# Performance work log

Measured on AMD Instinct MI355X. Metric: run time of the kernel, lower is better.

Reference implementation:

```python
import jax, jax.numpy as jnp
import numpy as np
import math

EPS = 1e-07
ALPHA = 0.2
FINAL_LAMBDA = 0.01   # final_beta in the original
ITERATIONS = 2
MEAN_DATA = 1.0

B, H, W, KH, KW, I, O, A = 16, 6, 6, 3, 3, 32, 32, 4


def setup_inputs() -> dict:
    key = jax.random.key(0)
    k1, k2 = jax.random.split(key)
    votes = jax.random.normal(k1, (B, H, W, KH, KW, I, O, A, A), dtype=jnp.float32)
    activations = jax.random.uniform(k2, (B, H, W, KH, KW, I, 1, 1, 1), dtype=jnp.float32)
    beta_a = jnp.full((1, 1, 1, 1, 1, 1, O, 1, 1), 0.5, dtype=jnp.float32)
    beta_u = jnp.full((1, 1, 1, 1, 1, 1, O, 1, 1), 0.5, dtype=jnp.float32)
    return {"votes": votes, "activations": activations, "beta_a": beta_a, "beta_u": beta_u}


def _m_step(a_i, V, R, R_prev, beta_a, beta_u, it_idx):
    # R mixing with previous assignments (faithful to source)
    R = R * a_i * (1.0 - ALPHA) + ALPHA * R_prev
    R_prev = R
    # reduce over kernel (3,4) and input-capsule (5) axes
    sum_R = jnp.sum(R, axis=(3, 4, 5), keepdims=True)                      # (b,h,w,1,1,1,o,1,1)
    mu = jnp.sum(R * V, axis=(3, 4, 5), keepdims=True) / (sum_R + EPS)     # (b,h,w,1,1,1,o,a,a)
    sigma_sq = jnp.sum(R * (V - mu) ** 2, axis=(3, 4, 5), keepdims=True) / (sum_R + EPS)
    cost_h = (beta_u - 0.5 * jnp.log(sigma_sq + EPS)) * sum_R / MEAN_DATA
    inv_temp = FINAL_LAMBDA * (1.0 - 0.95 ** (it_idx + 1))
    a_j = jax.nn.sigmoid(inv_temp * (beta_a - jnp.sum(cost_h, axis=(-1, -2), keepdims=True)))
    return mu, sigma_sq, a_j, R_prev


def _e_step_log(V, mu, sigma_sq, a_j):
    # log-space E-step: log N(V; mu, sigma) summed over the 4x4 pose entries
    log_p = -jnp.sum(jnp.log(2.0 * math.pi * sigma_sq + EPS) + (V - mu) ** 2 / (2.0 * sigma_sq),
                     axis=(-1, -2), keepdims=True)                         # (b,h,w,kh,kw,i,o,1,1)
    log_num = jnp.log(a_j + EPS) + log_p
    log_den = jax.scipy.special.logsumexp(log_num, axis=(3, 4, 6), keepdims=True)
    return jnp.exp(log_num - log_den)


def reference(votes, activations, beta_a, beta_u):
    b, h, w, kh, kw, i, o, a, _ = votes.shape
    # softmax over zeros along axis 6 -> uniform 1/o
    R = jnp.full((b, h, w, 1, 1, i, o, 1, 1), 1.0 / o, dtype=votes.dtype)
    R_prev = R
    mu = sigma_sq = a_j = None
    for it in range(ITERATIONS - 1):
        mu, sigma_sq, a_j, R_prev = _m_step(activations, votes, R, R_prev, beta_a, beta_u, it)
        R = _e_step_log(votes, mu, sigma_sq, a_j)
    # final M-step called with i = iterations (matches source)
    mu, sigma_sq, a_j, R_prev = _m_step(activations, votes, R, R_prev, beta_a, beta_u, ITERATIONS)
    poses = jnp.squeeze(mu, axis=(3, 4, 5))   # (b,h,w,o,a,a)
    acts = jnp.squeeze(a_j, axis=(3, 4, 5))   # (b,h,w,o,1,1)
    return poses, acts
```

## Files before the change

kernel.cpp:

```cpp
#include <hip/hip_runtime.h>


#define KKc 9
#define NIc 32
#define NOc 32
#define NAc 16
#define KIc 288
#define KOc 288
#define NPc 512
#define MSTR 17

__device__ __forceinline__ float wave_sum(float v) {
#pragma unroll
  for (int off = 32; off; off >>= 1) v += __shfl_down(v, off, 64);
  return v;
}
__device__ __forceinline__ float wave_max(float v) {
#pragma unroll
  for (int off = 32; off; off >>= 1) v = fmaxf(v, __shfl_down(v, off, 64));
  return v;
}

__global__ __launch_bounds__(256, 4)
void em_routing_kernel(const float* __restrict__ votes,
                       const float* __restrict__ acts_in,
                       const float* __restrict__ beta_a,
                       const float* __restrict__ beta_u,
                       float* __restrict__ out, int nsite)
{
  const int site = blockIdx.x;
  const int t    = threadIdx.x;
  const float EPSf  = 1e-7f;
  const float TWO_PI = 6.28318530717958647692f;

  __shared__ float s_VT[NAc * KOc];
  __shared__ float s_act[KIc];
  __shared__ float s_mu1[NOc * MSTR];
  __shared__ float s_lt1[NOc * MSTR];
  __shared__ float s_i2s[NOc * MSTR];
  __shared__ float s_m1v[NOc * MSTR];
  __shared__ float s_m1q[NOc * MSTR];
  __shared__ float s_laj[NOc];
  __shared__ float s_ln[KOc];
  __shared__ float s_w[KOc];
  __shared__ float s_sR2[NOc];
  __shared__ float s_red[4];
  __shared__ float s_red2[256];

  const float* vsite = votes + (size_t)site * (KIc * NPc);

  s_act[t] = acts_in[site * KIc + t];
  if (t < KIc - 256) s_act[t + 256] = acts_in[site * KIc + t + 256];
  __syncthreads();

  float sumR1;
  {
    float v = fmaf(0.8f, s_act[t], 0.2f);
    if (t < KIc - 256) v += fmaf(0.8f, s_act[t + 256], 0.2f);
    v = wave_sum(v);
    if ((t & 63) == 0) s_red[t >> 6] = v;
    __syncthreads();
    sumR1 = (s_red[0] + s_red[1] + s_red[2] + s_red[3]) * 0.03125f;
    __syncthreads();
  }

  float p1v0 = 0.f, p1v1 = 0.f, p1q0 = 0.f, p1q1 = 0.f;
#pragma unroll 4
  for (int ki = 0; ki < KIc; ++ki) {
    const float r = fmaf(0.8f, s_act[ki], 0.2f) * 0.03125f;
    const float2 v = *reinterpret_cast<const float2*>(vsite + ki * NPc + 2 * t);
    p1v0 = fmaf(r, v.x, p1v0);
    p1q0 = fmaf(r, v.x * v.x, p1q0);
    p1v1 = fmaf(r, v.y, p1v1);
    p1q1 = fmaf(r, v.y * v.y, p1q1);
  }
  {
    const int o1  = t >> 3;
    const int a2a = (t & 7) * 2;
    const float sR1e = sumR1 + EPSf;
    const float mua = p1v0 / sR1e;
    const float mub = p1v1 / sR1e;
    const float sga = fmaxf((p1q0 - mua * mua * (sumR1 + 2.f * EPSf)) / sR1e, 0.f);
    const float sgb = fmaxf((p1q1 - mub * mub * (sumR1 + 2.f * EPSf)) / sR1e, 0.f);
    const int b = o1 * MSTR + a2a;
    s_mu1[b]     = mua;  s_mu1[b + 1] = mub;
    s_lt1[b]     = logf(TWO_PI * sga + EPSf);
    s_lt1[b + 1] = logf(TWO_PI * sgb + EPSf);
    s_i2s[b]     = 0.5f / sga;
    s_i2s[b + 1] = 0.5f / sgb;
    s_m1v[b] = p1v0; s_m1v[b + 1] = p1v1;
    s_m1q[b] = p1q0; s_m1q[b + 1] = p1q1;
    const float bu = beta_u[o1];
    float ch = (bu - 0.5f * logf(sga + EPSf)) * sumR1
             + (bu - 0.5f * logf(sgb + EPSf)) * sumR1;
#pragma unroll
    for (int off = 1; off < 8; off <<= 1) ch += __shfl_xor(ch, off, 64);
    if ((t & 7) == 0) {
      const float aj = 1.f / (1.f + expf(-(0.0005f * (beta_a[o1] - ch))));
      s_laj[o1] = logf(aj + EPSf);
    }
  }
  __syncthreads();

  float sR2acc = 0.f;
  float m2va = 0.f, m2vb = 0.f, m2qa = 0.f, m2qb = 0.f;
  const int oB  = t & 31;
  const int a2B = (t >> 5) * 2;

  for (int i = 0; i < NIc; ++i) {
    __syncthreads();
    for (int idx = t; idx < KKc * 128; idx += 256) {
      const int kk  = idx >> 7;
      const int rem = idx & 127;
      const int o   = rem >> 2;
      const int a4  = (rem & 3) * 4;
      const float4 v = reinterpret_cast<const float4*>(vsite)[(kk * NIc + i) * 128 + rem];
      s_VT[(a4 + 0) * KOc + kk * NOc + o] = v.x;
      s_VT[(a4 + 1) * KOc + kk * NOc + o] = v.y;
      s_VT[(a4 + 2) * KOc + kk * NOc + o] = v.z;
      s_VT[(a4 + 3) * KOc + kk * NOc + o] = v.w;
    }
    __syncthreads();

    float ln1, ln2 = -1e30f;
    {
      const int o  = t & 31;
      const int ob = o * MSTR;
      float lp = 0.f;
#pragma unroll
      for (int a2 = 0; a2 < NAc; ++a2) {
        const float d = s_VT[a2 * KOc + t] - s_mu1[ob + a2];
        lp += s_lt1[ob + a2] + d * d * s_i2s[ob + a2];
      }
      ln1 = s_laj[o] - lp;
      s_ln[t] = ln1;
    }
    if (t < KOc - 256) {
      const int idx = t + 256;
      const int o   = idx & 31;
      const int ob  = o * MSTR;
      float lp = 0.f;
#pragma unroll
      for (int a2 = 0; a2 < NAc; ++a2) {
        const float d = s_VT[a2 * KOc + idx] - s_mu1[ob + a2];
        lp += s_lt1[ob + a2] + d * d * s_i2s[ob + a2];
      }
      ln2 = s_laj[o] - lp;
      s_ln[idx] = ln2;
    }
    float m = wave_max(fmaxf(ln1, ln2));
    if ((t & 63) == 0) s_red[t >> 6] = m;
    __syncthreads();
    m = fmaxf(fmaxf(s_red[0], s_red[1]), fmaxf(s_red[2], s_red[3]));
    float e = expf(ln1 - m) + ((t < KOc - 256) ? expf(ln2 - m) : 0.f);
    e = wave_sum(e);
    __syncthreads();
    if ((t & 63) == 0) s_red[t >> 6] = e;
    __syncthreads();
    const float logden = m + logf(s_red[0] + s_red[1] + s_red[2] + s_red[3]);

    {
      const int kk = t >> 5;
      s_w[t] = expf(ln1 - logden) * s_act[kk * NIc + i] * 0.8f;
    }
    if (t < KOc - 256) {
      const int idx = t + 256;
      const int kk  = idx >> 5;
      s_w[idx] = expf(ln2 - logden) * s_act[kk * NIc + i] * 0.8f;
    }
    __syncthreads();

    if (t < NOc) {
      float sw = 0.f;
#pragma unroll
      for (int kk = 0; kk < KKc; ++kk) sw += s_w[kk * NOc + t];
      sR2acc += sw;
    }
#pragma unroll
    for (int kk = 0; kk < KKc; ++kk) {
      const int bb = kk * NOc + oB;
      const float w  = s_w[bb];
      const float va = s_VT[a2B * KOc + bb];
      const float vb = s_VT[(a2B + 1) * KOc + bb];
      m2va = fmaf(w, va, m2va);
      m2qa = fmaf(w, va * va, m2qa);
      m2vb = fmaf(w, vb, m2vb);
      m2qb = fmaf(w, vb * vb, m2qb);
    }
  }

  if (t < NOc) s_sR2[t] = sR2acc;
  __syncthreads();

  {
    const float sumR = s_sR2[oB] + 0.2f * sumR1;
    const float sRe  = sumR + EPSf;
    const int b = oB * MSTR + a2B;
    const float Mva = m2va + 0.2f * s_m1v[b];
    const float Mqa = m2qa + 0.2f * s_m1q[b];
    const float Mvb = m2vb + 0.2f * s_m1v[b + 1];
    const float Mqb = m2qb + 0.2f * s_m1q[b + 1];
    const float mua = Mva / sRe;
    const float mub = Mvb / sRe;
    const float sga = fmaxf((Mqa - mua * mua * (sumR + 2.f * EPSf)) / sRe, 0.f);
    const float sgb = fmaxf((Mqb - mub * mub * (sumR + 2.f * EPSf)) / sRe, 0.f);

    float* poses = out + (size_t)site * NPc;
    poses[oB * NAc + a2B]     = mua;
    poses[oB * NAc + a2B + 1] = mub;

    const float bu = beta_u[oB];
    const float ch = (bu - 0.5f * logf(sga + EPSf)) * sumR
                   + (bu - 0.5f * logf(sgb + EPSf)) * sumR;
    s_red2[t] = ch;
  }
  __syncthreads();
  if (t < NOc) {
    float c = 0.f;
#pragma unroll
    for (int k = 0; k < 8; ++k) c += s_red2[t + 32 * k];
    const float aj = 1.f / (1.f + expf(-(0.00142625f * (beta_a[t] - c))));
    out[(size_t)nsite * NPc + site * NOc + t] = aj;
  }
}

extern "C" void kernel_launch(void* const* d_in, const int* in_sizes, int n_in,
                              void* d_out, int out_size, void* d_ws, size_t ws_size,
                              hipStream_t stream) {
  const float* votes  = (const float*)d_in[0];
  const float* acts   = (const float*)d_in[1];
  const float* beta_a = (const float*)d_in[2];
  const float* beta_u = (const float*)d_in[3];
  float* out = (float*)d_out;
  const int nsite = 16 * 6 * 6;
  em_routing_kernel<<<nsite, 256, 0, stream>>>(votes, acts, beta_a, beta_u, out, nsite);
}
```

Before: 594.8 us.

## Split EM routing into three kernels to parallelize across input capsules

The single per-site kernel becomes three launches. The first computes the first M-step statistics with four blocks per site. The second runs the E-step and partial second M-step with eight blocks per site, each handling four input capsules. The third reduces the partials and writes poses and activations. This raises grid size from 576 blocks to thousands so the GPU has more parallelism. It also folds the log-sigma term into a per-output base constant and changes the shared-memory vote layout to pair-major with padding. The cost is workspace traffic, two extra launches, and a second full read of the votes.

```diff
diff --git a/kernel.cpp b/kernel.cpp
--- a/kernel.cpp
+++ b/kernel.cpp
@@ -8,7 +8,11 @@
 #define KIc 288
 #define KOc 288
 #define NPc 512
-#define MSTR 17
+#define NSITE 576
+#define VSTR 17
+
+#define EPSf 1e-7f
+#define TWO_PIf 6.28318530717958647692f
 
 __device__ __forceinline__ float wave_sum(float v) {
 #pragma unroll
@@ -21,132 +25,138 @@
   return v;
 }
 
-__global__ __launch_bounds__(256, 4)
-void em_routing_kernel(const float* __restrict__ votes,
-                       const float* __restrict__ acts_in,
-                       const float* __restrict__ beta_a,
-                       const float* __restrict__ beta_u,
-                       float* __restrict__ out, int nsite)
+__global__ __launch_bounds__(128)
+void em_k1(const float* __restrict__ votes, const float* __restrict__ acts_in,
+           const float* __restrict__ beta_a, const float* __restrict__ beta_u,
+           float* __restrict__ w_mu1, float* __restrict__ w_i2s,
+           float* __restrict__ w_m1v, float* __restrict__ w_m1q,
+           float* __restrict__ w_base, float* __restrict__ w_sR1)
 {
-  const int site = blockIdx.x;
+  const int site = blockIdx.x >> 2;
+  const int qtr  = blockIdx.x & 3;
   const int t    = threadIdx.x;
-  const float EPSf  = 1e-7f;
-  const float TWO_PI = 6.28318530717958647692f;
-
-  __shared__ float s_VT[NAc * KOc];
+  const int p    = qtr * 128 + t;
+
   __shared__ float s_act[KIc];
-  __shared__ float s_mu1[NOc * MSTR];
-  __shared__ float s_lt1[NOc * MSTR];
-  __shared__ float s_i2s[NOc * MSTR];
-  __shared__ float s_m1v[NOc * MSTR];
-  __shared__ float s_m1q[NOc * MSTR];
-  __shared__ float s_laj[NOc];
-  __shared__ float s_ln[KOc];
+  __shared__ float s_red[2];
+
+  s_act[t] = acts_in[site * KIc + t];
+  s_act[t + 128] = acts_in[site * KIc + t + 128];
+  if (t < 32) s_act[t + 256] = acts_in[site * KIc + t + 256];
+  __syncthreads();
+
+  float v = fmaf(0.8f, s_act[t], 0.2f) + fmaf(0.8f, s_act[t + 128], 0.2f);
+  if (t < 32) v += fmaf(0.8f, s_act[t + 256], 0.2f);
+  v = wave_sum(v);
+  if ((t & 63) == 0) s_red[t >> 6] = v;
+  __syncthreads();
+  const float sumR1 = (s_red[0] + s_red[1]) * 0.03125f;
+
+  float pv = 0.f, pq = 0.f;
+  const float* vs = votes + (size_t)site * (KIc * NPc) + p;
+#pragma unroll 8
+  for (int ki = 0; ki < KIc; ++ki) {
+    const float r = fmaf(0.8f, s_act[ki], 0.2f) * 0.03125f;
+    const float x = vs[(size_t)ki * NPc];
+    pv = fmaf(r, x, pv);
+    pq = fmaf(r, x * x, pq);
+  }
+
+  const int o = p >> 4;
+  const float sR1e = sumR1 + EPSf;
+  const float mu = pv / sR1e;
+  const float sg = fmaxf((pq - mu * mu * (sumR1 + 2.f * EPSf)) / sR1e, 0.f);
+
+  w_mu1[(size_t)site * NPc + p] = mu;
+  w_i2s[(size_t)site * NPc + p] = 0.5f / sg;
+  w_m1v[(size_t)site * NPc + p] = pv;
+  w_m1q[(size_t)site * NPc + p] = pq;
+
+  float lt = logf(TWO_PIf * sg + EPSf);
+  float ch = (beta_u[o] - 0.5f * logf(sg + EPSf)) * sumR1;
+#pragma unroll
+  for (int off = 1; off < 16; off <<= 1) {
+    ch += __shfl_xor(ch, off, 64);
+    lt += __shfl_xor(lt, off, 64);
+  }
+  if ((t & 15) == 0) {
+    const float aj = 1.f / (1.f + expf(-(0.0005f * (beta_a[o] - ch))));
+    w_base[site * NOc + o] = logf(aj + EPSf) - lt;
+  }
+  if (t == 0) w_sR1[site] = sumR1;
+}
+
+__global__ __launch_bounds__(256)
+void em_k3(const float* __restrict__ votes, const float* __restrict__ acts_in,
+           const float* __restrict__ w_mu1, const float* __restrict__ w_i2s,
+           const float* __restrict__ w_base,
+           float* __restrict__ w_m2v, float* __restrict__ w_m2q,
+           float* __restrict__ w_sR2)
+{
+  const int site = blockIdx.x >> 3;
+  const int ig   = blockIdx.x & 7;
+  const int t    = threadIdx.x;
+
+  __shared__ float s_V[KOc * VSTR];
+  __shared__ float s_mu[NOc * VSTR];
+  __shared__ float s_is[NOc * VSTR];
+  __shared__ float s_base[NOc];
+  __shared__ float s_act[KIc];
   __shared__ float s_w[KOc];
-  __shared__ float s_sR2[NOc];
   __shared__ float s_red[4];
-  __shared__ float s_red2[256];
-
-  const float* vsite = votes + (size_t)site * (KIc * NPc);
-
+
+  for (int idx = t; idx < NPc; idx += 256) {
+    const int o = idx >> 4, a2 = idx & 15;
+    s_mu[o * VSTR + a2] = w_mu1[(size_t)site * NPc + idx];
+    s_is[o * VSTR + a2] = w_i2s[(size_t)site * NPc + idx];
+  }
+  if (t < NOc) s_base[t] = w_base[site * NOc + t];
   s_act[t] = acts_in[site * KIc + t];
   if (t < KIc - 256) s_act[t + 256] = acts_in[site * KIc + t + 256];
-  __syncthreads();
-
-  float sumR1;
-  {
-    float v = fmaf(0.8f, s_act[t], 0.2f);
-    if (t < KIc - 256) v += fmaf(0.8f, s_act[t + 256], 0.2f);
-    v = wave_sum(v);
-    if ((t & 63) == 0) s_red[t >> 6] = v;
-    __syncthreads();
-    sumR1 = (s_red[0] + s_red[1] + s_red[2] + s_red[3]) * 0.03125f;
-    __syncthreads();
-  }
-
-  float p1v0 = 0.f, p1v1 = 0.f, p1q0 = 0.f, p1q1 = 0.f;
-#pragma unroll 4
-  for (int ki = 0; ki < KIc; ++ki) {
-    const float r = fmaf(0.8f, s_act[ki], 0.2f) * 0.03125f;
-    const float2 v = *reinterpret_cast<const float2*>(vsite + ki * NPc + 2 * t);
-    p1v0 = fmaf(r, v.x, p1v0);
-    p1q0 = fmaf(r, v.x * v.x, p1q0);
-    p1v1 = fmaf(r, v.y, p1v1);
-    p1q1 = fmaf(r, v.y * v.y, p1q1);
-  }
-  {
-    const int o1  = t >> 3;
-    const int a2a = (t & 7) * 2;
-    const float sR1e = sumR1 + EPSf;
-    const float mua = p1v0 / sR1e;
-    const float mub = p1v1 / sR1e;
-    const float sga = fmaxf((p1q0 - mua * mua * (sumR1 + 2.f * EPSf)) / sR1e, 0.f);
-    const float sgb = fmaxf((p1q1 - mub * mub * (sumR1 + 2.f * EPSf)) / sR1e, 0.f);
-    const int b = o1 * MSTR + a2a;
-    s_mu1[b]     = mua;  s_mu1[b + 1] = mub;
-    s_lt1[b]     = logf(TWO_PI * sga + EPSf);
-    s_lt1[b + 1] = logf(TWO_PI * sgb + EPSf);
-    s_i2s[b]     = 0.5f / sga;
-    s_i2s[b + 1] = 0.5f / sgb;
-    s_m1v[b] = p1v0; s_m1v[b + 1] = p1v1;
-    s_m1q[b] = p1q0; s_m1q[b + 1] = p1q1;
-    const float bu = beta_u[o1];
-    float ch = (bu - 0.5f * logf(sga + EPSf)) * sumR1
-             + (bu - 0.5f * logf(sgb + EPSf)) * sumR1;
-#pragma unroll
-    for (int off = 1; off < 8; off <<= 1) ch += __shfl_xor(ch, off, 64);
-    if ((t & 7) == 0) {
-      const float aj = 1.f / (1.f + expf(-(0.0005f * (beta_a[o1] - ch))));
-      s_laj[o1] = logf(aj + EPSf);
-    }
-  }
-  __syncthreads();
-
-  float sR2acc = 0.f;
-  float m2va = 0.f, m2vb = 0.f, m2qa = 0.f, m2qb = 0.f;
+
+  const float4* vsite4 = reinterpret_cast<const float4*>(votes + (size_t)site * (KIc * NPc));
+
+  float m2va = 0.f, m2vb = 0.f, m2qa = 0.f, m2qb = 0.f, sR2acc = 0.f;
   const int oB  = t & 31;
   const int a2B = (t >> 5) * 2;
 
-  for (int i = 0; i < NIc; ++i) {
-    __syncthreads();
-    for (int idx = t; idx < KKc * 128; idx += 256) {
+  for (int ii = 0; ii < 4; ++ii) {
+    const int i = ig * 4 + ii;
+    __syncthreads();
+    for (int idx = t; idx < 1152; idx += 256) {
       const int kk  = idx >> 7;
       const int rem = idx & 127;
-      const int o   = rem >> 2;
-      const int a4  = (rem & 3) * 4;
-      const float4 v = reinterpret_cast<const float4*>(vsite)[(kk * NIc + i) * 128 + rem];
-      s_VT[(a4 + 0) * KOc + kk * NOc + o] = v.x;
-      s_VT[(a4 + 1) * KOc + kk * NOc + o] = v.y;
-      s_VT[(a4 + 2) * KOc + kk * NOc + o] = v.z;
-      s_VT[(a4 + 3) * KOc + kk * NOc + o] = v.w;
+      const int pair = kk * NOc + (rem >> 2);
+      const int a4   = (rem & 3) * 4;
+      const float4 x = vsite4[(size_t)(kk * NIc + i) * 128 + rem];
+      s_V[pair * VSTR + a4 + 0] = x.x;
+      s_V[pair * VSTR + a4 + 1] = x.y;
+      s_V[pair * VSTR + a4 + 2] = x.z;
+      s_V[pair * VSTR + a4 + 3] = x.w;
     }
     __syncthreads();
 
     float ln1, ln2 = -1e30f;
     {
-      const int o  = t & 31;
-      const int ob = o * MSTR;
+      const int o = t & 31;
       float lp = 0.f;
 #pragma unroll
       for (int a2 = 0; a2 < NAc; ++a2) {
-        const float d = s_VT[a2 * KOc + t] - s_mu1[ob + a2];
-        lp += s_lt1[ob + a2] + d * d * s_i2s[ob + a2];
+        const float d = s_V[t * VSTR + a2] - s_mu[o * VSTR + a2];
+        lp = fmaf(d * d, s_is[o * VSTR + a2], lp);
       }
-      ln1 = s_laj[o] - lp;
-      s_ln[t] = ln1;
+      ln1 = s_base[o] - lp;
     }
     if (t < KOc - 256) {
       const int idx = t + 256;
-      const int o   = idx & 31;
-      const int ob  = o * MSTR;
+      const int o = idx & 31;
       float lp = 0.f;
 #pragma unroll
       for (int a2 = 0; a2 < NAc; ++a2) {
-        const float d = s_VT[a2 * KOc + idx] - s_mu1[ob + a2];
-        lp += s_lt1[ob + a2] + d * d * s_i2s[ob + a2];
+        const float d = s_V[idx * VSTR + a2] - s_mu[o * VSTR + a2];
+        lp = fmaf(d * d, s_is[o * VSTR + a2], lp);
       }
-      ln2 = s_laj[o] - lp;
-      s_ln[idx] = ln2;
+      ln2 = s_base[o] - lp;
     }
     float m = wave_max(fmaxf(ln1, ln2));
     if ((t & 63) == 0) s_red[t >> 6] = m;
@@ -159,15 +169,9 @@
     __syncthreads();
     const float logden = m + logf(s_red[0] + s_red[1] + s_red[2] + s_red[3]);
 
-    {
-      const int kk = t >> 5;
-      s_w[t] = expf(ln1 - logden) * s_act[kk * NIc + i] * 0.8f;
-    }
-    if (t < KOc - 256) {
-      const int idx = t + 256;
-      const int kk  = idx >> 5;
-      s_w[idx] = expf(ln2 - logden) * s_act[kk * NIc + i] * 0.8f;
-    }
+    s_w[t] = expf(ln1 - logden) * s_act[(t >> 5) * NIc + i] * 0.8f;
+    if (t < KOc - 256)
+      s_w[t + 256] = expf(ln2 - logden) * s_act[8 * NIc + i] * 0.8f;
     __syncthreads();
 
     if (t < NOc) {
@@ -180,8 +184,8 @@
     for (int kk = 0; kk < KKc; ++kk) {
       const int bb = kk * NOc + oB;
       const float w  = s_w[bb];
-      const float va = s_VT[a2B * KOc + bb];
-      const float vb = s_VT[(a2B + 1) * KOc + bb];
+      const float va = s_V[bb * VSTR + a2B];
+      const float vb = s_V[bb * VSTR + a2B + 1];
       m2va = fmaf(w, va, m2va);
       m2qa = fmaf(w, va * va, m2qa);
       m2vb = fmaf(w, vb, m2vb);
@@ -189,38 +193,68 @@
     }
   }
 
-  if (t < NOc) s_sR2[t] = sR2acc;
-  __syncthreads();
-
-  {
-    const float sumR = s_sR2[oB] + 0.2f * sumR1;
-    const float sRe  = sumR + EPSf;
-    const int b = oB * MSTR + a2B;
-    const float Mva = m2va + 0.2f * s_m1v[b];
-    const float Mqa = m2qa + 0.2f * s_m1q[b];
-    const float Mvb = m2vb + 0.2f * s_m1v[b + 1];
-    const float Mqb = m2qb + 0.2f * s_m1q[b + 1];
-    const float mua = Mva / sRe;
-    const float mub = Mvb / sRe;
-    const float sga = fmaxf((Mqa - mua * mua * (sumR + 2.f * EPSf)) / sRe, 0.f);
-    const float sgb = fmaxf((Mqb - mub * mub * (sumR + 2.f * EPSf)) / sRe, 0.f);
-
-    float* poses = out + (size_t)site * NPc;
-    poses[oB * NAc + a2B]     = mua;
-    poses[oB * NAc + a2B + 1] = mub;
-
-    const float bu = beta_u[oB];
-    const float ch = (bu - 0.5f * logf(sga + EPSf)) * sumR
-                   + (bu - 0.5f * logf(sgb + EPSf)) * sumR;
-    s_red2[t] = ch;
-  }
+  reinterpret_cast<float2*>(w_m2v)[(size_t)blockIdx.x * 256 + t] = make_float2(m2va, m2vb);
+  reinterpret_cast<float2*>(w_m2q)[(size_t)blockIdx.x * 256 + t] = make_float2(m2qa, m2qb);
+  if (t < NOc) w_sR2[(size_t)blockIdx.x * NOc + t] = sR2acc;
+}
+
+__global__ __launch_bounds__(256)
+void em_k4(const float* __restrict__ beta_a, const float* __restrict__ beta_u,
+           const float* __restrict__ w_m1v, const float* __restrict__ w_m1q,
+           const float* __restrict__ w_sR1,
+           const float* __restrict__ w_m2v, const float* __restrict__ w_m2q,
+           const float* __restrict__ w_sR2,
+           float* __restrict__ out)
+{
+  const int site = blockIdx.x;
+  const int t    = threadIdx.x;
+  const int oB   = t & 31;
+  const int a2B  = (t >> 5) * 2;
+
+  __shared__ float s_R[NOc];
+  __shared__ float s_c[256];
+
+  float Mva = 0.f, Mvb = 0.f, Mqa = 0.f, Mqb = 0.f, sR2 = 0.f;
+#pragma unroll
+  for (int g = 0; g < 8; ++g) {
+    const size_t blk = (size_t)site * 8 + g;
+    const float2 v = reinterpret_cast<const float2*>(w_m2v)[blk * 256 + t];
+    const float2 q = reinterpret_cast<const float2*>(w_m2q)[blk * 256 + t];
+    Mva += v.x; Mvb += v.y; Mqa += q.x; Mqb += q.y;
+    if (t < NOc) sR2 += w_sR2[blk * NOc + t];
+  }
+  if (t < NOc) s_R[t] = sR2;
+  __syncthreads();
+
+  const float sumR1 = w_sR1[site];
+  const float sumR  = s_R[oB] + 0.2f * sumR1;
+  const float sRe   = sumR + EPSf;
+  const int p = oB * NAc + a2B;
+
+  Mva += 0.2f * w_m1v[(size_t)site * NPc + p];
+  Mqa += 0.2f * w_m1q[(size_t)site * NPc + p];
+  Mvb += 0.2f * w_m1v[(size_t)site * NPc + p + 1];
+  Mqb += 0.2f * w_m1q[(size_t)site * NPc + p + 1];
+
+  const float mua = Mva / sRe;
+  const float mub = Mvb / sRe;
+  const float sga = fmaxf((Mqa - mua * mua * (sumR + 2.f * EPSf)) / sRe, 0.f);
+  const float sgb = fmaxf((Mqb - mub * mub * (sumR + 2.f * EPSf)) / sRe, 0.f);
+
+  float* poses = out + (size_t)site * NPc;
+  poses[p]     = mua;
+  poses[p + 1] = mub;
+
+  const float bu = beta_u[oB];
+  s_c[t] = (bu - 0.5f * logf(sga + EPSf)) * sumR
+         + (bu - 0.5f * logf(sgb + EPSf)) * sumR;
   __syncthreads();
   if (t < NOc) {
     float c = 0.f;
 #pragma unroll
-    for (int k = 0; k < 8; ++k) c += s_red2[t + 32 * k];
+    for (int k = 0; k < 8; ++k) c += s_c[t + 32 * k];
     const float aj = 1.f / (1.f + expf(-(0.00142625f * (beta_a[t] - c))));
-    out[(size_t)nsite * NPc + site * NOc + t] = aj;
+    out[(size_t)NSITE * NPc + site * NOc + t] = aj;
   }
 }
 
@@ -232,6 +266,23 @@
   const float* beta_a = (const float*)d_in[2];
   const float* beta_u = (const float*)d_in[3];
   float* out = (float*)d_out;
-  const int nsite = 16 * 6 * 6;
-  em_routing_kernel<<<nsite, 256, 0, stream>>>(votes, acts, beta_a, beta_u, out, nsite);
-}
+
+  float* ws = (float*)d_ws;
+  const size_t SP = (size_t)NSITE * NPc;
+  float* w_mu1  = ws;
+  float* w_i2s  = ws + SP;
+  float* w_m1v  = ws + 2 * SP;
+  float* w_m1q  = ws + 3 * SP;
+  float* w_base = ws + 4 * SP;
+  float* w_sR1  = w_base + NSITE * NOc;
+  float* w_m2v  = w_sR1 + 1024;
+  float* w_m2q  = w_m2v + (size_t)4608 * NPc;
+  float* w_sR2  = w_m2q + (size_t)4608 * NPc;
+
+  em_k1<<<NSITE * 4, 128, 0, stream>>>(votes, acts, beta_a, beta_u,
+                                       w_mu1, w_i2s, w_m1v, w_m1q, w_base, w_sR1);
+  em_k3<<<NSITE * 8, 256, 0, stream>>>(votes, acts, w_mu1, w_i2s, w_base,
+                                       w_m2v, w_m2q, w_sR2);
+  em_k4<<<NSITE, 256, 0, stream>>>(beta_a, beta_u, w_m1v, w_m1q, w_sR1,
+                                   w_m2v, w_m2q, w_sR2, out);
+}
```

Result: faster. 562.2 us (-5.5%).
